# Kernel tuning notes

Hardware: AMD Instinct MI355X
Metric: run time of the kernel (lower is better)

The kernel has to match this reference:

```python
import jax, jax.numpy as jnp
import numpy as np

N_ORDER = 256      # HiPPO order (window_size=[256])
OUT_LEN = 96       # output_window_size
IN_LEN = 720       # input_window_size
MULTISCALE = [1, 2, 4]
MODES = 32         # min(32, min(OUT_LEN, IN_LEN)//2)
EPS = 1e-5


def _transition(N):
    Q = np.arange(N, dtype=np.float64)
    R = (2 * Q + 1)[:, None]
    j, i = np.meshgrid(Q, Q)
    A = np.where(i < j, -1.0, (-1.0) ** (i - j + 1)) * R
    B = (-1.0) ** Q[:, None] * R
    return A, B


def _bilinear_discretize(A, B, dt):
    # scipy cont2discrete(method='bilinear'): Ad = (I - dt/2 A)^-1 (I + dt/2 A), Bd = (I - dt/2 A)^-1 dt B
    n = A.shape[0]
    I = np.eye(n)
    ima = I - 0.5 * dt * A
    Ad = np.linalg.solve(ima, I + 0.5 * dt * A)
    Bd = np.linalg.solve(ima, dt * B)
    return Ad, Bd.squeeze(-1)


def _eval_legendre(N, x):
    # Legendre P_n(x), n=0..N-1, via three-term recurrence. Returns [len(x), N].
    P = np.zeros((N, x.shape[0]))
    P[0] = 1.0
    if N > 1:
        P[1] = x
    for n in range(1, N - 1):
        P[n + 1] = ((2 * n + 1) * x * P[n] - n * P[n - 1]) / (n + 1)
    return P.T


def setup_inputs() -> dict:
    key = jax.random.key(0)
    ks = jax.random.split(key, 4)
    B, L, E = 16, IN_LEN, 64
    x = jax.random.normal(ks[0], (B, L, E), dtype=jnp.float32)
    scale = 1.0 / (N_ORDER * N_ORDER)
    wr = scale * jax.random.uniform(ks[1], (3, N_ORDER, N_ORDER, MODES), dtype=jnp.float32)
    wi = scale * jax.random.uniform(ks[2], (3, N_ORDER, N_ORDER, MODES), dtype=jnp.float32)
    mlp_w = 0.1 * jax.random.normal(ks[3], (1, 3), dtype=jnp.float32)
    mlp_b = jnp.zeros((1,), dtype=jnp.float32)
    A_c, B_c = _transition(N_ORDER)
    Ads, Bds, evs = [], [], []
    for m in MULTISCALE:
        dt = 1.0 / OUT_LEN / m
        Ad, Bd = _bilinear_discretize(A_c, B_c, dt)
        vals = np.arange(0.0, 1.0, dt)
        ev = _eval_legendre(N_ORDER, 1.0 - 2.0 * vals)  # [m*OUT_LEN, N]
        Ads.append(Ad); Bds.append(Bd); evs.append(ev[-OUT_LEN:])
    A = jnp.asarray(np.stack(Ads), dtype=jnp.float32)          # [3,N,N]
    Bv = jnp.asarray(np.stack(Bds), dtype=jnp.float32)         # [3,N]
    eval_last = jnp.asarray(np.stack(evs), dtype=jnp.float32)  # [3,OUT_LEN,N]
    return {"x": x, "wr": wr, "wi": wi, "mlp_w": mlp_w, "mlp_b": mlp_b,
            "A": A, "Bv": Bv, "eval_last": eval_last}


def _hippo(xin, Ad, Bd):
    # xin: [B,E,T] -> states [B,E,N,T]; c_t = A c_{t-1} + B f_t
    c0 = jnp.zeros(xin.shape[:2] + (Ad.shape[0],), xin.dtype)
    def step(c, f):  # f: [B,E]
        c = c @ Ad.T + f[..., None] * Bd
        return c, c
    _, cs = jax.lax.scan(step, c0, jnp.moveaxis(xin, -1, 0))  # [T,B,E,N]
    return jnp.transpose(cs, (1, 2, 3, 0))


def _spec_conv(xc, wr, wi):
    # xc: [B,E,N,T]; FFT -> low-mode complex channel mix -> iFFT
    T = xc.shape[-1]
    x_ft = jnp.fft.rfft(xc)                 # [B,E,N,T//2+1]
    a = x_ft[..., :MODES]
    w = (wr + 1j * wi).astype(a.dtype)      # [N,N,MODES]
    out = jnp.einsum('bjix,iox->bjox', a, w)
    nf = T // 2 + 1
    out_ft = jnp.pad(out, ((0, 0), (0, 0), (0, 0), (0, nf - MODES)))
    return jnp.fft.irfft(out_ft, n=T)       # [B,E,N,T]


def reference(x, wr, wi, mlp_w, mlp_b, A, Bv, eval_last):
    # instance standard scale (RevIN-style, no affine)
    mean = jnp.mean(x, axis=1, keepdims=True)            # [B,1,E]
    std = jnp.sqrt(jnp.var(x, axis=1, keepdims=True) + EPS)
    xn = (x - mean) / std
    xe = jnp.transpose(xn, (0, 2, 1))                    # [B,E,L]
    decs = []
    for s, m in enumerate(MULTISCALE):
        T = m * OUT_LEN
        x_in = xe[:, :, -T:]
        xc = _hippo(x_in, A[s], Bv[s])                   # [B,E,N,T]
        out1 = _spec_conv(xc, wr[s], wi[s])              # [B,E,N,T]
        x_dec_c = out1[:, :, :, OUT_LEN - 1]             # [B,E,N]  (input >= output branch, jump_dist=0)
        decs.append(x_dec_c @ eval_last[s].T)            # [B,E,OUT_LEN]
    xd = jnp.stack(decs, axis=-1)                        # [B,E,OUT,3]
    xd = (xd @ mlp_w.T + mlp_b)[..., 0]                  # [B,E,OUT]
    xd = jnp.transpose(xd, (0, 2, 1))                    # [B,OUT,E]
    return xd * std + mean
```

## Files before the change

kernel.cpp:

```cpp
#include <hip/hip_runtime.h>

typedef unsigned short u16;
typedef unsigned int u32;

typedef __bf16 bf16x8 __attribute__((ext_vector_type(8)));
typedef unsigned short ushort8 __attribute__((ext_vector_type(8)));
typedef float f32x16 __attribute__((ext_vector_type(16)));

#define STATSP 2048
#define EPOFF 32768
#define KKOFF0 591872
#define KKOFF1 616448
#define KKOFF2 665600
#define WOFF 763904
#define R0OFF 5482496
#define R1OFF 6072320
#define R2OFF 7251968
#define HTOTOFF 11675648
#define AD64 0
#define PD64 196608
#define KKD64 589824

__device__ __forceinline__ u32 pack_hl(float a) {
  u32 bits = __builtin_bit_cast(u32, a);
  u32 hi = (bits + 0x7fffu + ((bits >> 16) & 1u)) >> 16;
  float hif = __builtin_bit_cast(float, hi << 16);
  float r = a - hif;
  u32 lo = __builtin_bit_cast(u32, r) >> 16;
  return hi | (lo << 16);
}

__device__ __forceinline__ void unpk8(const u32* p, bf16x8& h, bf16x8& l) {
  ushort8 hu, lu;
#pragma unroll
  for (int j = 0; j < 8; ++j) {
    u32 v = p[j];
    hu[j] = (unsigned short)(v & 0xffffu);
    lu[j] = (unsigned short)(v >> 16);
  }
  h = __builtin_bit_cast(bf16x8, hu);
  l = __builtin_bit_cast(bf16x8, lu);
}

__device__ __forceinline__ void gload_lds16(const float* g, float* l) {
  __builtin_amdgcn_global_load_lds(
      (const __attribute__((address_space(1))) void*)g,
      (__attribute__((address_space(3))) void*)l, 16, 0, 0);
}

__global__ __launch_bounds__(256) void k_pre(const float* __restrict__ Ab,
                                             const float* __restrict__ Bb,
                                             const float* __restrict__ xin,
                                             const float* __restrict__ ev,
                                             float* __restrict__ ws) {
  __shared__ float rs[4][64], rq[4][64];
  int blk = blockIdx.x, tid = threadIdx.x;
  if (blk < 771) {
    double* dws = (double*)(ws + WOFF);
    int idx = blk * 256 + tid;
    if (idx < 196608) {
      dws[AD64 + idx] = (double)Ab[idx];
    } else {
      int g = idx - 196608;
      const int rowoff[3] = {0, 24576, 73728};
      const int kko[3] = {KKOFF0, KKOFF1, KKOFF2};
      int s = g >> 8, i = g & 255;
      float v = Bb[g];
      dws[KKD64 + rowoff[s] + i] = (double)v;
      ((u32*)ws)[kko[s] + i] = pack_hl(v);
    }
  } else if (blk < 963) {
    int b2 = blk - 771;
    int b = b2 / 12, part = b2 % 12;
    int j = tid & 63, g = tid >> 6;
    const float* xp = xin + ((size_t)b * 720 + part * 60 + g) * 64 + j;
    float sum = 0.f, ss = 0.f;
#pragma unroll
    for (int i = 0; i < 15; ++i) {
      float v = xp[(size_t)i * 256];
      sum += v; ss += v * v;
    }
    rs[g][j] = sum; rq[g][j] = ss;
    __syncthreads();
    if (g == 0) {
      float s = rs[0][j] + rs[1][j] + rs[2][j] + rs[3][j];
      float q = rq[0][j] + rq[1][j] + rq[2][j] + rq[3][j];
      float* dst = ws + STATSP + ((size_t)b2 * 64 + j) * 2;
      dst[0] = s; dst[1] = q;
    }
  } else if (blk < 987) {
    int idx = (blk - 963) * 256 + tid;
    for (; idx < 36864; idx += 24 * 256) ws[HTOTOFF + idx] = 0.f;
  } else {
    int idx = (blk - 987) * 256 + tid;
    u32 ph = pack_hl(ev[idx]);
    u16* eb = (u16*)((u32*)ws + EPOFF);
    eb[idx] = (u16)(ph & 0xffffu);
    eb[73728 + idx] = (u16)(ph >> 16);
  }
}

struct G64Jobs {
  const double* A[8]; const double* B[8]; double* C[8]; float* CF[8];
  int M[8]; int transB[8]; int tile0[8];
  int njobs;
};

__global__ __launch_bounds__(256) void k_gemm64(G64Jobs jb) {
  int bid = blockIdx.x;
  int j = 0;
  for (int q = 1; q < jb.njobs; ++q) if (bid >= jb.tile0[q]) j = q;
  int local = bid - jb.tile0[j];
  int tm = local >> 3, tn = local & 7;
  const double* A = jb.A[j];
  const double* Bm = jb.B[j];
  double* C = jb.C[j];
  float* CF = jb.CF[j];
  int M = jb.M[j], tB = jb.transB[j];
  int row0 = tm * 32, col0 = tn * 32;
  __shared__ double As[32][33], Bs[32][33];
  int tid = threadIdx.x;
  int ty = tid >> 4, tx = tid & 15;
  int lr = tid >> 3, lk = (tid & 7) << 2;
  double va[4], vb[4];
#pragma unroll
  for (int u = 0; u < 4; ++u) {
    va[u] = (row0 + lr < M) ? A[(size_t)(row0 + lr) * 256 + lk + u] : 0.0;
    vb[u] = tB ? Bm[(size_t)(col0 + lr) * 256 + lk + u]
               : Bm[(size_t)lr * 256 + col0 + lk + u];
  }
  double a00 = 0., a01 = 0., a10 = 0., a11 = 0.;
  for (int kc = 0; kc < 256; kc += 32) {
#pragma unroll
    for (int u = 0; u < 4; ++u) {
      As[lr][lk + u] = va[u];
      if (tB) Bs[lk + u][lr] = vb[u];
      else    Bs[lr][lk + u] = vb[u];
    }
    __syncthreads();
    if (kc < 224) {
      int kn = kc + 32;
#pragma unroll
      for (int u = 0; u < 4; ++u) {
        va[u] = (row0 + lr < M) ? A[(size_t)(row0 + lr) * 256 + kn + lk + u] : 0.0;
        vb[u] = tB ? Bm[(size_t)(col0 + lr) * 256 + kn + lk + u]
                   : Bm[(size_t)(kn + lr) * 256 + col0 + lk + u];
      }
    }
#pragma unroll 8
    for (int k = 0; k < 32; ++k) {
      double x0 = As[2 * ty][k], x1 = As[2 * ty + 1][k];
      double y0 = Bs[k][2 * tx], y1 = Bs[k][2 * tx + 1];
      a00 = fma(x0, y0, a00); a01 = fma(x0, y1, a01);
      a10 = fma(x1, y0, a10); a11 = fma(x1, y1, a11);
    }
    __syncthreads();
  }
  int r0 = row0 + 2 * ty, c0 = col0 + 2 * tx;
  if (r0 < M) {
    C[(size_t)r0 * 256 + c0] = a00; C[(size_t)r0 * 256 + c0 + 1] = a01;
    if (CF) {
      ((u32*)CF)[(size_t)r0 * 256 + c0] = pack_hl((float)a00);
      ((u32*)CF)[(size_t)r0 * 256 + c0 + 1] = pack_hl((float)a01);
    }
  }
  if (r0 + 1 < M) {
    C[(size_t)(r0 + 1) * 256 + c0] = a10; C[(size_t)(r0 + 1) * 256 + c0 + 1] = a11;
    if (CF) {
      ((u32*)CF)[(size_t)(r0 + 1) * 256 + c0] = pack_hl((float)a10);
      ((u32*)CF)[(size_t)(r0 + 1) * 256 + c0 + 1] = pack_hl((float)a11);
    }
  }
}

__global__ __launch_bounds__(384, 5) void k_s3(const float* __restrict__ wr,
                                               const float* __restrict__ wi,
                                               float* __restrict__ ws) {
  __shared__ float stage[2][2048];
  __shared__ u32 pairs[3 * 1056];
  int bid = blockIdx.x;
  int jidx = bid >> 7;
  int r127 = bid & 127;
  int mb = ((r127 & 7) << 4) | (r127 >> 3);
  int s = jidx >> 1, p = jidx & 1;
  const float* w = (p ? wi : wr) + (size_t)s * 2097152;
  const u16* ebase = (const u16*)((const u32*)ws + EPOFF);
  const u16* eh = ebase + (size_t)s * 24576;
  const u16* el = ebase + 73728 + (size_t)s * 24576;
  int i0 = mb * 2;
  int tid = threadIdx.x;
  int lane = tid & 63;
  int wid = tid >> 6;
  int il = wid & 1, f = wid >> 1;

  int tcol = lane & 31;
  int og8 = (lane >> 5) << 3;
  const u16* bhp = eh + (size_t)(f * 32 + tcol) * 256 + og8;
  const u16* blp = el + (size_t)(f * 32 + tcol) * 256 + og8;

  bool stager = (wid < 4);
  int sq0 = wid * 2;
  int s_i[2], s_o[2], s_x[2];
#pragma unroll
  for (int j = 0; j < 2; ++j) {
    int qq = sq0 + j;
    s_i[j] = qq >> 2;
    s_o[j] = (qq & 3) * 8 + (lane >> 3);
    s_x[j] = (lane & 7) * 4;
  }

  f32x16 acc;
#pragma unroll
  for (int r = 0; r < 16; ++r) acc[r] = 0.f;

  if (stager) {
#pragma unroll
    for (int j = 0; j < 2; ++j) {
      const float* g = w + (((size_t)(i0 + s_i[j]) * 256 + s_o[j]) << 5) + s_x[j];
      gload_lds16(g, &stage[0][(sq0 + j) * 256]);
    }
  }
  __syncthreads();

#pragma unroll 2
  for (int c = 0; c < 8; ++c) {
    int buf = c & 1;
    if (c < 7 && stager) {
      int kon = (c + 1) * 32;
#pragma unroll
      for (int j = 0; j < 2; ++j) {
        const float* g = w + (((size_t)(i0 + s_i[j]) * 256 + kon + s_o[j]) << 5) + s_x[j];
        gload_lds16(g, &stage[buf ^ 1][(sq0 + j) * 256]);
      }
    }
    int ko = c * 32;
#pragma unroll
    for (int ks = 0; ks < 2; ++ks) {
      int ob = ks * 16 + og8;
      float fa[8];
#pragma unroll
      for (int j = 0; j < 8; ++j)
        fa[j] = stage[buf][il * 1024 + (ob + j) * 32 + tcol];
      bf16x8 ah, al;
#pragma unroll
      for (int j = 0; j < 8; ++j) {
        __bf16 h = (__bf16)fa[j];
        ah[j] = h;
        al[j] = (__bf16)(fa[j] - (float)h);
      }
      bf16x8 bh = *(const bf16x8*)(bhp + ko + ks * 16);
      bf16x8 bl = *(const bf16x8*)(blp + ko + ks * 16);
      acc = __builtin_amdgcn_mfma_f32_32x32x16_bf16(ah, bh, acc, 0, 0, 0);
      acc = __builtin_amdgcn_mfma_f32_32x32x16_bf16(ah, bl, acc, 0, 0, 0);
      acc = __builtin_amdgcn_mfma_f32_32x32x16_bf16(al, bh, acc, 0, 0, 0);
    }
    __syncthreads();
  }

  int x0 = (lane >> 5) << 2;
  u32 mine[16];
#pragma unroll
  for (int r = 0; r < 16; ++r) mine[r] = pack_hl(acc[r]);
  if (il == 0) {
#pragma unroll
    for (int r = 0; r < 16; ++r) {
      int row = x0 + (r & 3) + ((r >> 2) << 3);
      pairs[f * 1056 + row * 33 + tcol] = mine[r];
    }
  }
  __syncthreads();
  if (il == 1) {
    u32* W2 = (u32*)(ws + WOFF) + (size_t)jidx * 786432 +
              (size_t)(mb >> 2) * 24576 + ((mb & 3) << 1);
#pragma unroll
    for (int r = 0; r < 16; ++r) {
      int row = x0 + (r & 3) + ((r >> 2) << 3);
      uint2 st;
      st.x = pairs[f * 1056 + row * 33 + tcol];
      st.y = mine[r];
      *(uint2*)(W2 + (size_t)(row * 96 + f * 32 + tcol) * 8) = st;
    }
  }
}

__global__ __launch_bounds__(256) void k_s4(float* __restrict__ ws) {
  int bid = blockIdx.x;
  const int cums[6] = {0, 36, 72, 144, 216, 360};
  int jidx = 0;
#pragma unroll
  for (int q = 1; q < 6; ++q) if (bid >= cums[q]) jidx = q;
  int local = bid - cums[jidx];
  int s = jidx >> 1, p = jidx & 1;
  const int Ts[3] = {96, 192, 384};
  const int KKo[3] = {KKOFF0, KKOFF1, KKOFF2};
  const int Ro[3] = {R0OFF, R1OFF, R2OFF};
  int T = Ts[s];
  int td = local / 12, tn = local % 12;
  int d0 = td * 32;
  int tid = threadIdx.x;
  int lane = tid & 63, wid = tid >> 6;
  int n0 = tn * 256 + wid * 64;
  int l31 = lane & 31, kg = lane >> 5;
  const u32* Ap = (const u32*)ws + KKo[s] + (size_t)(d0 + l31) * 256 + kg * 8;
  const u32* Bp = (const u32*)ws + WOFF + (size_t)jidx * 786432 + (size_t)kg * 24576;
  const u32* b0p = Bp + (size_t)(n0 + l31) * 8;
  const u32* b1p = Bp + (size_t)(n0 + 32 + l31) * 8;
  float* C = ws + Ro[s] + (size_t)p * T * 3072;

  f32x16 acc0, acc1;
#pragma unroll
  for (int r = 0; r < 16; ++r) { acc0[r] = 0.f; acc1[r] = 0.f; }

#pragma unroll 2
  for (int ks = 0; ks < 16; ++ks) {
    uint4 a0 = *(const uint4*)(Ap + ks * 16);
    uint4 a1 = *(const uint4*)(Ap + ks * 16 + 4);
    size_t bo = (size_t)ks * 49152;
    uint4 x0 = *(const uint4*)(b0p + bo);
    uint4 x1 = *(const uint4*)(b0p + bo + 4);
    uint4 y0 = *(const uint4*)(b1p + bo);
    uint4 y1 = *(const uint4*)(b1p + bo + 4);
    u32 ap[8] = {a0.x, a0.y, a0.z, a0.w, a1.x, a1.y, a1.z, a1.w};
    bf16x8 ah, al;
    unpk8(ap, ah, al);
    {
      u32 bp[8] = {x0.x, x0.y, x0.z, x0.w, x1.x, x1.y, x1.z, x1.w};
      bf16x8 bh, bl;
      unpk8(bp, bh, bl);
      acc0 = __builtin_amdgcn_mfma_f32_32x32x16_bf16(ah, bh, acc0, 0, 0, 0);
      acc0 = __builtin_amdgcn_mfma_f32_32x32x16_bf16(ah, bl, acc0, 0, 0, 0);
      acc0 = __builtin_amdgcn_mfma_f32_32x32x16_bf16(al, bh, acc0, 0, 0, 0);
      acc0 = __builtin_amdgcn_mfma_f32_32x32x16_bf16(al, bl, acc0, 0, 0, 0);
    }
    {
      u32 bp[8] = {y0.x, y0.y, y0.z, y0.w, y1.x, y1.y, y1.z, y1.w};
      bf16x8 bh, bl;
      unpk8(bp, bh, bl);
      acc1 = __builtin_amdgcn_mfma_f32_32x32x16_bf16(ah, bh, acc1, 0, 0, 0);
      acc1 = __builtin_amdgcn_mfma_f32_32x32x16_bf16(ah, bl, acc1, 0, 0, 0);
      acc1 = __builtin_amdgcn_mfma_f32_32x32x16_bf16(al, bh, acc1, 0, 0, 0);
      acc1 = __builtin_amdgcn_mfma_f32_32x32x16_bf16(al, bl, acc1, 0, 0, 0);
    }
  }

  int crow = kg << 2;
#pragma unroll
  for (int r = 0; r < 16; ++r) {
    int row = d0 + crow + (r & 3) + ((r >> 2) << 3);
    C[(size_t)row * 3072 + n0 + l31] = acc0[r];
    C[(size_t)row * 3072 + n0 + 32 + l31] = acc1[r];
  }
}

__global__ __launch_bounds__(192) void k_s5a(const float* __restrict__ mlpw, float* __restrict__ ws) {
  int bid = blockIdx.x;
  int s = bid >> 7;
  int rem = bid & 127;
  int x = rem >> 2;
  int tq = rem & 3;
  const int Ts[3] = {96, 192, 384};
  const int Ro[3] = {R0OFF, R1OFF, R2OFF};
  const int lpbase[3] = {288, 192, 0};
  int T = Ts[s];
  int Lc = T >> 3;
  __shared__ float cs[384][2];
  __shared__ float Lsr[8][24], Lsi[8][24];
  int tid = threadIdx.x;
  for (int e = tid; e < T; e += 192) {
    float th = 6.283185307179586f * (float)e / (float)T;
    cs[e][0] = cosf(th);
    cs[e][1] = sinf(th);
  }
  int c = tid / 24, tl = tid % 24;
  int t = tq * 24 + tl;
  const float* Rre = ws + Ro[s] + (size_t)x * 96 + t;
  const float* Rim = Rre + (size_t)T * 3072;
  float* Htot = ws + HTOTOFF;
  float wsc = mlpw[s];
  __syncthreads();
  int d0 = c * Lc;
  float zr = 0.f, zi = 0.f;
  for (int d = d0; d < d0 + Lc; ++d) {
    float rr = Rre[(size_t)d * 3072];
    float ri = Rim[(size_t)d * 3072];
    int e1 = (x * d) % T;
    float c1 = cs[e1][0], s1 = cs[e1][1];
    zr += c1 * rr + s1 * ri;
    zi += c1 * ri - s1 * rr;
  }
  Lsr[c][tl] = zr; Lsi[c][tl] = zi;
  __syncthreads();
  if (c == 0) {
    float pr = 0.f, pi = 0.f;
#pragma unroll
    for (int cc = 0; cc < 8; ++cc) {
      float lr = Lsr[cc][tl], li = Lsi[cc][tl];
      Lsr[cc][tl] = pr; Lsi[cc][tl] = pi;
      pr += lr; pi += li;
    }
  }
  __syncthreads();
  zr = Lsr[c][tl]; zi = Lsi[c][tl];
  float sc = (((x == 0) ? 1.f : 2.f) / (float)T) * wsc;
  for (int d = d0; d < d0 + Lc; ++d) {
    float rr = Rre[(size_t)d * 3072];
    float ri = Rim[(size_t)d * 3072];
    int e1 = (x * d) % T;
    float c1 = cs[e1][0], s1 = cs[e1][1];
    zr += c1 * rr + s1 * ri;
    zi += c1 * ri - s1 * rr;
    int k = T - 1 - d;
    int e2 = (x * (95 - k)) % T;
    if (e2 < 0) e2 += T;
    float c2 = cs[e2][0], s2 = cs[e2][1];
    atomicAdd(Htot + (size_t)(lpbase[s] + k) * 96 + t, sc * (c2 * zr - s2 * zi));
  }
}

__global__ __launch_bounds__(256) void k_s6(const float* __restrict__ xin, const float* __restrict__ mlpb_p,
                                            const float* __restrict__ ws, float* __restrict__ out) {
  int b = blockIdx.x >> 2, tq = blockIdx.x & 3;
  int tid = threadIdx.x;
  int j = tid & 63, tsub = tid >> 6;
  __shared__ float Ht[384 * 24];
  for (int idx = tid; idx < 384 * 24; idx += 256) {
    int lp = idx / 24, c = idx % 24;
    Ht[idx] = ws[HTOTOFF + lp * 96 + tq * 24 + c];
  }
  float ssum = 0.f, sq = 0.f;
#pragma unroll
  for (int p = 0; p < 12; ++p) {
    const float* src = ws + STATSP + (((size_t)b * 12 + p) * 64 + j) * 2;
    ssum += src[0]; sq += src[1];
  }
  float mn = ssum * (1.f / 720.f);
  float var = sq * (1.f / 720.f) - mn * mn;
  float sd = sqrtf(var + 1e-5f);
  __syncthreads();
  float mlpb = mlpb_p[0];
  float acc[6] = {0.f, 0.f, 0.f, 0.f, 0.f, 0.f};
  float accS[6] = {0.f, 0.f, 0.f, 0.f, 0.f, 0.f};
  const float* xp = xin + ((size_t)b * 720 + 336) * 64 + j;
  for (int lp = 0; lp < 384; ++lp) {
    float xv = xp[(size_t)lp * 64];
    const float* hr = &Ht[lp * 24 + tsub * 6];
    float2 h01 = *(const float2*)&hr[0];
    float2 h23 = *(const float2*)&hr[2];
    float2 h45 = *(const float2*)&hr[4];
    float hh[6] = {h01.x, h01.y, h23.x, h23.y, h45.x, h45.y};
#pragma unroll
    for (int u = 0; u < 6; ++u) {
      acc[u] += xv * hh[u];
      accS[u] += hh[u];
    }
  }
#pragma unroll
  for (int u = 0; u < 6; ++u) {
    int t = tq * 24 + tsub * 6 + u;
    float val = acc[u] + mn * (1.f - accS[u]) + sd * mlpb;
    out[((size_t)b * 96 + t) * 64 + j] = val;
  }
}

extern "C" void kernel_launch(void* const* d_in, const int* in_sizes, int n_in,
                              void* d_out, int out_size, void* d_ws, size_t ws_size,
                              hipStream_t stream) {
  const float* x  = (const float*)d_in[0];
  const float* wr = (const float*)d_in[1];
  const float* wi = (const float*)d_in[2];
  const float* mw = (const float*)d_in[3];
  const float* mb = (const float*)d_in[4];
  const float* Ab = (const float*)d_in[5];
  const float* Bb = (const float*)d_in[6];
  const float* ev = (const float*)d_in[7];
  float* wsf = (float*)d_ws;
  float* out = (float*)d_out;

  k_pre<<<1275, 256, 0, stream>>>(Ab, Bb, x, ev, wsf);

  const double* AD = (const double*)(wsf + WOFF) + AD64;
  double* PD = (double*)(wsf + WOFF) + PD64;
  double* KD = (double*)(wsf + WOFF) + KKD64;
  static const int Ts[3] = {96, 192, 384};
  static const int rowoff[3] = {0, 24576, 73728};
  static const int KKo[3] = {KKOFF0, KKOFF1, KKOFF2};

  int have[3] = {1, 1, 1};
  for (int r = 0; r <= 8; ++r) {
    G64Jobs jb;
    jb.njobs = 0;
    int tiles = 0;
    for (int s = 0; s < 3; ++s) {
      int T = Ts[s];
      if (have[s] >= T) continue;
      const double* Pn = (r == 0) ? (AD + (size_t)s * 65536)
                                  : (PD + (size_t)(2 * s + (r & 1)) * 65536);
      int M = ((2 * have[s] < T) ? 2 * have[s] : T) - have[s];
      int q = jb.njobs++;
      jb.A[q] = KD + rowoff[s]; jb.B[q] = Pn;
      jb.C[q] = KD + rowoff[s] + (size_t)have[s] * 256;
      jb.CF[q] = wsf + KKo[s] + (size_t)have[s] * 256;
      jb.M[q] = M; jb.transB[q] = 1; jb.tile0[q] = tiles;
      tiles += ((M + 31) / 32) * 8;
      if (2 * have[s] < T) {
        q = jb.njobs++;
        jb.A[q] = Pn; jb.B[q] = Pn;
        jb.C[q] = PD + (size_t)(2 * s + ((r + 1) & 1)) * 65536;
        jb.CF[q] = nullptr;
        jb.M[q] = 256; jb.transB[q] = 0; jb.tile0[q] = tiles;
        tiles += 64;
      }
      have[s] = (2 * have[s] < T) ? 2 * have[s] : T;
    }
    if (jb.njobs) k_gemm64<<<tiles, 256, 0, stream>>>(jb);
  }

  k_s3<<<768, 384, 0, stream>>>(wr, wi, wsf);
  k_s4<<<504, 256, 0, stream>>>(wsf);
  k_s5a<<<384, 192, 0, stream>>>(mw, wsf);
  k_s6<<<64, 256, 0, stream>>>(x, mb, wsf, out);
}
```

Measured before the change: 372.8 us.

## Split-K the fp64 power-chain GEMMs with atomic accumulation and a separate pack pass

The fp64 doubling-chain GEMMs, which build powers of A and the Krylov rows, now split K into four chunks of 64 and accumulate with atomic adds. This gives four times as many blocks and removes the per-block K loop. Destinations therefore have to be pre-zeroed, so the power buffers move to a triple-buffer rotation with in-chain zero jobs, and k_pre gets extra zeroing blocks. The bf16 hi/lo packing of the Krylov rows moves out of the GEMM epilogue into a separate k_pack kernel. The trade-off is extra atomic traffic, zeroing work, one more launch, and a summation order that is no longer deterministic.

```diff
diff --git a/kernel.cpp b/kernel.cpp
--- a/kernel.cpp
+++ b/kernel.cpp
@@ -19,7 +19,7 @@
 #define HTOTOFF 11675648
 #define AD64 0
 #define PD64 196608
-#define KKD64 589824
+#define KKD64 786432
 
 __device__ __forceinline__ u32 pack_hl(float a) {
   u32 bits = __builtin_bit_cast(u32, a);
@@ -63,11 +63,8 @@
     } else {
       int g = idx - 196608;
       const int rowoff[3] = {0, 24576, 73728};
-      const int kko[3] = {KKOFF0, KKOFF1, KKOFF2};
       int s = g >> 8, i = g & 255;
-      float v = Bb[g];
-      dws[KKD64 + rowoff[s] + i] = (double)v;
-      ((u32*)ws)[kko[s] + i] = pack_hl(v);
+      dws[KKD64 + rowoff[s] + i] = (double)Bb[g];
     }
   } else if (blk < 963) {
     int b2 = blk - 771;
@@ -91,86 +88,105 @@
   } else if (blk < 987) {
     int idx = (blk - 963) * 256 + tid;
     for (; idx < 36864; idx += 24 * 256) ws[HTOTOFF + idx] = 0.f;
-  } else {
+  } else if (blk < 1275) {
     int idx = (blk - 987) * 256 + tid;
     u32 ph = pack_hl(ev[idx]);
     u16* eb = (u16*)((u32*)ws + EPOFF);
     eb[idx] = (u16)(ph & 0xffffu);
     eb[73728 + idx] = (u16)(ph >> 16);
-  }
-}
-
-struct G64Jobs {
-  const double* A[8]; const double* B[8]; double* C[8]; float* CF[8];
-  int M[8]; int transB[8]; int tile0[8];
+  } else if (blk < 1467) {
+    int g0 = ((blk - 1275) * 256 + tid) * 4;
+    int s = g0 >> 16, off = g0 & 65535;
+    double* dst = (double*)(ws + WOFF) + PD64 + (size_t)(s * 3) * 65536 + off;
+    dst[0] = 0.; dst[1] = 0.; dst[2] = 0.; dst[3] = 0.;
+  } else {
+    int g0 = ((blk - 1467) * 256 + tid) * 4;
+    int local = (g0 < 24576) ? g0 : (g0 < 73728 ? g0 - 24576 : g0 - 73728);
+    if (local >= 256) {
+      double* dst = (double*)(ws + WOFF) + KKD64 + g0;
+      dst[0] = 0.; dst[1] = 0.; dst[2] = 0.; dst[3] = 0.;
+    }
+  }
+}
+
+struct CJobs {
+  const double* A[12]; const double* B[12]; double* C[12];
+  int M[12]; int transB[12]; int tile0[12];
   int njobs;
 };
 
-__global__ __launch_bounds__(256) void k_gemm64(G64Jobs jb) {
+__global__ __launch_bounds__(256) void k_chain(CJobs jb) {
   int bid = blockIdx.x;
   int j = 0;
   for (int q = 1; q < jb.njobs; ++q) if (bid >= jb.tile0[q]) j = q;
   int local = bid - jb.tile0[j];
-  int tm = local >> 3, tn = local & 7;
+  int tB = jb.transB[j];
+  int tid = threadIdx.x;
+  if (tB == 2) {
+    double* Z = jb.C[j] + (size_t)local * 1024 + tid * 4;
+    Z[0] = 0.; Z[1] = 0.; Z[2] = 0.; Z[3] = 0.;
+    return;
+  }
+  int M = jb.M[j];
   const double* A = jb.A[j];
   const double* Bm = jb.B[j];
   double* C = jb.C[j];
-  float* CF = jb.CF[j];
-  int M = jb.M[j], tB = jb.transB[j];
-  int row0 = tm * 32, col0 = tn * 32;
-  __shared__ double As[32][33], Bs[32][33];
-  int tid = threadIdx.x;
+  int kq = local & 3, tn = (local >> 2) & 7, tm = local >> 5;
+  int row0 = tm * 32, col0 = tn * 32, k0 = kq * 64;
+  __shared__ double As[32][65];
+  __shared__ double Bs[64][33];
+  {
+    int r = tid >> 3, k8 = (tid & 7) << 3;
+    if (row0 + r < M) {
+      const double* src = A + (size_t)(row0 + r) * 256 + k0 + k8;
+#pragma unroll
+      for (int u = 0; u < 8; ++u) As[r][k8 + u] = src[u];
+    } else {
+#pragma unroll
+      for (int u = 0; u < 8; ++u) As[r][k8 + u] = 0.0;
+    }
+  }
+  if (tB == 0) {
+    int k = tid >> 2, c8 = (tid & 3) << 3;
+    const double* src = Bm + (size_t)(k0 + k) * 256 + col0 + c8;
+#pragma unroll
+    for (int u = 0; u < 8; ++u) Bs[k][c8 + u] = src[u];
+  } else {
+    int c = tid >> 3, k8 = (tid & 7) << 3;
+    const double* src = Bm + (size_t)(col0 + c) * 256 + k0 + k8;
+#pragma unroll
+    for (int u = 0; u < 8; ++u) Bs[k8 + u][c] = src[u];
+  }
+  __syncthreads();
   int ty = tid >> 4, tx = tid & 15;
-  int lr = tid >> 3, lk = (tid & 7) << 2;
-  double va[4], vb[4];
-#pragma unroll
-  for (int u = 0; u < 4; ++u) {
-    va[u] = (row0 + lr < M) ? A[(size_t)(row0 + lr) * 256 + lk + u] : 0.0;
-    vb[u] = tB ? Bm[(size_t)(col0 + lr) * 256 + lk + u]
-               : Bm[(size_t)lr * 256 + col0 + lk + u];
-  }
   double a00 = 0., a01 = 0., a10 = 0., a11 = 0.;
-  for (int kc = 0; kc < 256; kc += 32) {
-#pragma unroll
-    for (int u = 0; u < 4; ++u) {
-      As[lr][lk + u] = va[u];
-      if (tB) Bs[lk + u][lr] = vb[u];
-      else    Bs[lr][lk + u] = vb[u];
-    }
-    __syncthreads();
-    if (kc < 224) {
-      int kn = kc + 32;
-#pragma unroll
-      for (int u = 0; u < 4; ++u) {
-        va[u] = (row0 + lr < M) ? A[(size_t)(row0 + lr) * 256 + kn + lk + u] : 0.0;
-        vb[u] = tB ? Bm[(size_t)(col0 + lr) * 256 + kn + lk + u]
-                   : Bm[(size_t)(kn + lr) * 256 + col0 + lk + u];
-      }
-    }
 #pragma unroll 8
-    for (int k = 0; k < 32; ++k) {
-      double x0 = As[2 * ty][k], x1 = As[2 * ty + 1][k];
-      double y0 = Bs[k][2 * tx], y1 = Bs[k][2 * tx + 1];
-      a00 = fma(x0, y0, a00); a01 = fma(x0, y1, a01);
-      a10 = fma(x1, y0, a10); a11 = fma(x1, y1, a11);
-    }
-    __syncthreads();
+  for (int k = 0; k < 64; ++k) {
+    double x0 = As[2 * ty][k], x1 = As[2 * ty + 1][k];
+    double y0 = Bs[k][2 * tx], y1 = Bs[k][2 * tx + 1];
+    a00 = fma(x0, y0, a00); a01 = fma(x0, y1, a01);
+    a10 = fma(x1, y0, a10); a11 = fma(x1, y1, a11);
   }
   int r0 = row0 + 2 * ty, c0 = col0 + 2 * tx;
   if (r0 < M) {
-    C[(size_t)r0 * 256 + c0] = a00; C[(size_t)r0 * 256 + c0 + 1] = a01;
-    if (CF) {
-      ((u32*)CF)[(size_t)r0 * 256 + c0] = pack_hl((float)a00);
-      ((u32*)CF)[(size_t)r0 * 256 + c0 + 1] = pack_hl((float)a01);
-    }
+    __hip_atomic_fetch_add(&C[(size_t)r0 * 256 + c0], a00, __ATOMIC_RELAXED, __HIP_MEMORY_SCOPE_AGENT);
+    __hip_atomic_fetch_add(&C[(size_t)r0 * 256 + c0 + 1], a01, __ATOMIC_RELAXED, __HIP_MEMORY_SCOPE_AGENT);
   }
   if (r0 + 1 < M) {
-    C[(size_t)(r0 + 1) * 256 + c0] = a10; C[(size_t)(r0 + 1) * 256 + c0 + 1] = a11;
-    if (CF) {
-      ((u32*)CF)[(size_t)(r0 + 1) * 256 + c0] = pack_hl((float)a10);
-      ((u32*)CF)[(size_t)(r0 + 1) * 256 + c0 + 1] = pack_hl((float)a11);
-    }
-  }
+    __hip_atomic_fetch_add(&C[(size_t)(r0 + 1) * 256 + c0], a10, __ATOMIC_RELAXED, __HIP_MEMORY_SCOPE_AGENT);
+    __hip_atomic_fetch_add(&C[(size_t)(r0 + 1) * 256 + c0 + 1], a11, __ATOMIC_RELAXED, __HIP_MEMORY_SCOPE_AGENT);
+  }
+}
+
+__global__ __launch_bounds__(256) void k_pack(float* __restrict__ ws) {
+  int idx = blockIdx.x * 256 + threadIdx.x;
+  const double* KD = (const double*)(ws + WOFF) + KKD64;
+  const int kko[3] = {KKOFF0, KKOFF1, KKOFF2};
+  int s, local;
+  if (idx < 24576) { s = 0; local = idx; }
+  else if (idx < 73728) { s = 1; local = idx - 24576; }
+  else { s = 2; local = idx - 73728; }
+  ((u32*)ws)[kko[s] + local] = pack_hl((float)KD[idx]);
 }
 
 __global__ __launch_bounds__(384, 5) void k_s3(const float* __restrict__ wr,
@@ -476,45 +492,50 @@
   float* wsf = (float*)d_ws;
   float* out = (float*)d_out;
 
-  k_pre<<<1275, 256, 0, stream>>>(Ab, Bb, x, ev, wsf);
+  k_pre<<<1635, 256, 0, stream>>>(Ab, Bb, x, ev, wsf);
 
   const double* AD = (const double*)(wsf + WOFF) + AD64;
   double* PD = (double*)(wsf + WOFF) + PD64;
   double* KD = (double*)(wsf + WOFF) + KKD64;
   static const int Ts[3] = {96, 192, 384};
   static const int rowoff[3] = {0, 24576, 73728};
-  static const int KKo[3] = {KKOFF0, KKOFF1, KKOFF2};
 
   int have[3] = {1, 1, 1};
   for (int r = 0; r <= 8; ++r) {
-    G64Jobs jb;
+    CJobs jb;
     jb.njobs = 0;
     int tiles = 0;
     for (int s = 0; s < 3; ++s) {
       int T = Ts[s];
       if (have[s] >= T) continue;
       const double* Pn = (r == 0) ? (AD + (size_t)s * 65536)
-                                  : (PD + (size_t)(2 * s + (r & 1)) * 65536);
+                                  : (PD + (size_t)(s * 3 + (r - 1) % 3) * 65536);
       int M = ((2 * have[s] < T) ? 2 * have[s] : T) - have[s];
       int q = jb.njobs++;
       jb.A[q] = KD + rowoff[s]; jb.B[q] = Pn;
       jb.C[q] = KD + rowoff[s] + (size_t)have[s] * 256;
-      jb.CF[q] = wsf + KKo[s] + (size_t)have[s] * 256;
       jb.M[q] = M; jb.transB[q] = 1; jb.tile0[q] = tiles;
-      tiles += ((M + 31) / 32) * 8;
+      tiles += ((M + 31) / 32) * 32;
       if (2 * have[s] < T) {
         q = jb.njobs++;
         jb.A[q] = Pn; jb.B[q] = Pn;
-        jb.C[q] = PD + (size_t)(2 * s + ((r + 1) & 1)) * 65536;
-        jb.CF[q] = nullptr;
+        jb.C[q] = PD + (size_t)(s * 3 + r % 3) * 65536;
         jb.M[q] = 256; jb.transB[q] = 0; jb.tile0[q] = tiles;
-        tiles += 64;
+        tiles += 256;
+        if (4 * have[s] < T) {
+          q = jb.njobs++;
+          jb.A[q] = nullptr; jb.B[q] = nullptr;
+          jb.C[q] = PD + (size_t)(s * 3 + (r + 1) % 3) * 65536;
+          jb.M[q] = 0; jb.transB[q] = 2; jb.tile0[q] = tiles;
+          tiles += 64;
+        }
       }
       have[s] = (2 * have[s] < T) ? 2 * have[s] : T;
     }
-    if (jb.njobs) k_gemm64<<<tiles, 256, 0, stream>>>(jb);
-  }
-
+    if (jb.njobs) k_chain<<<tiles, 256, 0, stream>>>(jb);
+  }
+
+  k_pack<<<672, 256, 0, stream>>>(wsf);
   k_s3<<<768, 384, 0, stream>>>(wr, wi, wsf);
   k_s4<<<504, 256, 0, stream>>>(wsf);
   k_s5a<<<384, 192, 0, stream>>>(mw, wsf);
```

Result: faster. 330.4 us (-11.4%).
